# Performance work log

Measured on AMD Instinct MI355X. Metric: run time of the kernel, lower is better.

## Reference

```python
import jax, jax.numpy as jnp
import numpy as np


def setup_inputs() -> dict:
    key = jax.random.key(0)
    k0, k1, k2, k3 = jax.random.split(key, 4)
    H = 256  # hidden_dim_size
    DK = 256
    DV = 256
    hidden_states = jax.random.normal(k0, (1, 32, H, 16, 16), dtype=jnp.float32)
    # torch nn.Linear(H, dk, bias=False) computes x @ W.T; we store W.T directly as (H, dk)
    Wq = jax.random.normal(k1, (H, DK), dtype=jnp.float32) * (1.0 / np.sqrt(H))
    Wk = jax.random.normal(k2, (H, DK), dtype=jnp.float32) * (1.0 / np.sqrt(H))
    Wv = jax.random.normal(k3, (H, DV), dtype=jnp.float32) * (1.0 / np.sqrt(H))
    return {"hidden_states": hidden_states, "Wq": Wq, "Wk": Wk, "Wv": Wv}


def reference(hidden_states, Wq, Wk, Wv):
    # (b, t, c, h, w) -> (b, t, h, w, c)
    x = jnp.transpose(hidden_states, (0, 1, 3, 4, 2))
    nb, nt, nr, nc, nh = x.shape
    xf = x.reshape(-1, nh)  # (N, H) with N = b*t*h*w
    q = xf @ Wq             # (N, dk)
    k = xf @ Wk             # (N, dk)
    v = xf @ Wv             # (N, dv)
    dk = Wq.shape[1]
    scores = (q @ k.T) / jnp.sqrt(jnp.asarray(dk, dtype=q.dtype))  # (N, N)
    attn = jax.nn.softmax(scores, axis=-1) @ v                     # (N, dv)
    out = attn.reshape(nb, nt, nr, nc, -1)
    return jnp.transpose(out, (0, 1, 4, 2, 3))  # (b, t, dv, h, w)
```

## Files before the change

kernel.cpp:

```cpp
#include <hip/hip_runtime.h>
#include <stdint.h>

typedef __attribute__((ext_vector_type(8))) short bh8;
typedef __attribute__((ext_vector_type(4))) float f32x4;
typedef __attribute__((ext_vector_type(16))) float f32x16;
typedef __attribute__((ext_vector_type(2))) __fp16 h16x2;
typedef unsigned int uint32;

__device__ __forceinline__ unsigned short f2bf(float f) {
  uint32 u = __builtin_bit_cast(uint32, f);
  u += 0x7fffu + ((u >> 16) & 1u);
  return (unsigned short)(u >> 16);
}

__device__ __forceinline__ uint32 cvtpk_bf16(float lo, float hi) {
  uint32 r;
  asm("v_cvt_pk_bf16_f32 %0, %1, %2" : "=v"(r) : "v"(lo), "v"(hi));
  return r;
}

__device__ __forceinline__ float exp2_hw(float x) {
  float r;
  asm("v_exp_f32 %0, %1" : "=v"(r) : "v"(x));
  return r;
}

__device__ __forceinline__ float max3f(float a, float b, float c) {
  return fmaxf(fmaxf(a, b), c);
}

__device__ __forceinline__ void lds_load16(const void* g, void* l) {
  auto gp = (const __attribute__((address_space(1))) uint32*)(uintptr_t)(g);
  auto lp = (__attribute__((address_space(3))) uint32*)(uintptr_t)(l);
  __builtin_amdgcn_global_load_lds(gp, lp, 16, 0, 0);
}

__global__ __launch_bounds__(256) void k_transpose(
    const float* __restrict__ hidden, const float* __restrict__ Wq,
    const float* __restrict__ Wk, const float* __restrict__ Wv,
    unsigned short* __restrict__ xb, unsigned short* __restrict__ wt) {
  int bid = blockIdx.x, c0 = blockIdx.y * 16, tid = threadIdx.x;
  const float* in; unsigned short* out; float scale = 1.0f;
  if (bid < 32) { in = hidden + (size_t)bid * 65536; out = xb + (size_t)bid * 65536; }
  else {
    int j = bid - 32;
    in = (j == 0) ? Wq : (j == 1 ? Wk : Wv);
    out = wt + (size_t)j * 65536;
    if (j == 0) scale = 0.0625f * 1.4426950408889634f;
  }
  __shared__ uint32 lt[256 * 9];
  uint32 pk[8];
#pragma unroll
  for (int i = 0; i < 8; ++i) {
    float a = in[(size_t)(c0 + 2 * i) * 256 + tid] * scale;
    float b = in[(size_t)(c0 + 2 * i + 1) * 256 + tid] * scale;
    pk[i] = (uint32)f2bf(a) | ((uint32)f2bf(b) << 16);
  }
#pragma unroll
  for (int i = 0; i < 8; ++i) lt[tid * 9 + i] = pk[i];
  __syncthreads();
  int q2 = tid & 1;
#pragma unroll
  for (int rr = 0; rr < 2; ++rr) {
    int r = rr * 128 + (tid >> 1);
    uint4 v;
    v.x = lt[r * 9 + q2 * 4 + 0]; v.y = lt[r * 9 + q2 * 4 + 1];
    v.z = lt[r * 9 + q2 * 4 + 2]; v.w = lt[r * 9 + q2 * 4 + 3];
    *(uint4*)(out + (size_t)r * 256 + c0 + q2 * 8) = v;
  }
}

__global__ __launch_bounds__(256, 2) void k_gemm(
    const unsigned short* __restrict__ xb, const unsigned short* __restrict__ wt,
    unsigned short* __restrict__ qb, unsigned short* __restrict__ kb,
    unsigned short* __restrict__ vtb) {
  __shared__ char lds[32768];
  char* ldsA = lds; char* ldsB = lds + 16384;
  int tid = threadIdx.x, z = blockIdx.z;
  int l = tid & 63, w = tid >> 6, g = l >> 4, r15 = l & 15;
  int wr = w >> 1, wc = w & 1;
  const unsigned short *Ag, *Bg; unsigned short* out;
  int arow0, brow0; size_t ostride;
  if (z < 2) {
    Ag = xb; arow0 = blockIdx.x * 128;
    Bg = wt + (size_t)z * 65536; brow0 = blockIdx.y * 128;
    out = z ? kb : qb; ostride = 256;
  } else {
    Ag = wt + 2 * 65536; arow0 = blockIdx.y * 128;
    Bg = xb; brow0 = blockIdx.x * 128;
    out = vtb; ostride = 8192;
  }
  f32x4 acc[4][4];
#pragma unroll
  for (int i = 0; i < 4; ++i)
#pragma unroll
    for (int j = 0; j < 4; ++j) acc[i][j] = (f32x4){0.f, 0.f, 0.f, 0.f};

  for (int kk = 0; kk < 4; ++kk) {
    int c0 = kk * 64;
    __syncthreads();
#pragma unroll
    for (int p = 0; p < 4; ++p) {
      int off = p * 4096 + tid * 16;
      int row = off >> 7, ch = (off >> 4) & 7, sc = ch ^ (row & 7);
      lds_load16((const char*)Ag + ((size_t)(arow0 + row) * 256 + c0) * 2 + sc * 16, ldsA + off);
    }
#pragma unroll
    for (int p = 0; p < 4; ++p) {
      int off = p * 4096 + tid * 16;
      int row = off >> 7, ch = (off >> 4) & 7, sc = ch ^ (row & 7);
      lds_load16((const char*)Bg + ((size_t)(brow0 + row) * 256 + c0) * 2 + sc * 16, ldsB + off);
    }
    __syncthreads();
#pragma unroll
    for (int ks = 0; ks < 2; ++ks) {
      bh8 af[4], bfr[4];
#pragma unroll
      for (int i = 0; i < 4; ++i) {
        int rowa = wr * 64 + i * 16 + r15;
        af[i] = *(const bh8*)(ldsA + rowa * 128 + (((ks * 4 + g) ^ (rowa & 7)) * 16));
        int rowb = wc * 64 + i * 16 + r15;
        bfr[i] = *(const bh8*)(ldsB + rowb * 128 + (((ks * 4 + g) ^ (rowb & 7)) * 16));
      }
#pragma unroll
      for (int i = 0; i < 4; ++i)
#pragma unroll
        for (int j = 0; j < 4; ++j)
          acc[i][j] = __builtin_amdgcn_mfma_f32_16x16x32_bf16(af[i], bfr[j], acc[i][j], 0, 0, 0);
    }
  }
  __syncthreads();
#pragma unroll
  for (int i = 0; i < 4; ++i)
#pragma unroll
    for (int j = 0; j < 4; ++j)
#pragma unroll
      for (int r = 0; r < 4; ++r) {
        int rowl = wr * 64 + i * 16 + g * 4 + r;
        int coll = wc * 64 + j * 16 + r15;
        *(unsigned short*)(lds + rowl * 256 + coll * 2) = f2bf(acc[i][j][r]);
      }
  __syncthreads();
#pragma unroll
  for (int p = 0; p < 8; ++p) {
    int off = p * 4096 + tid * 16;
    int row = off >> 8, colb = off & 255;
    *(uint4*)((char*)out + ((size_t)(arow0 + row) * ostride + (size_t)brow0) * 2 + colb) =
        *(const uint4*)(lds + off);
  }
}

__global__ __launch_bounds__(512, 2) void k_attn(
    const unsigned short* __restrict__ qg, const unsigned short* __restrict__ kg,
    const unsigned short* __restrict__ vtg, uint32* __restrict__ Op,
    float* __restrict__ mp, float* __restrict__ lp, int S, int shift, int KS) {
  extern __shared__ char smem[];
  int tid = threadIdx.x;
  int w = tid >> 6, l = tid & 63, col = l & 31, half = l >> 5;
  int bid = blockIdx.x;
  int s = bid & (S - 1);
  int qb = bid >> shift;
  int qrow0 = qb * 256 + w * 32;

  int nt = KS >> 6, kb0 = s * KS;

  auto stage = [&](int buf, int kvb) {
    char* Kd = smem + buf * 65536;
    char* Vd = Kd + 32768;
#pragma unroll
    for (int p = 0; p < 4; ++p) {
      int off = p * 8192 + tid * 16;
      int row = off >> 9, ch = (off >> 4) & 31;
      lds_load16((const char*)kg + (size_t)(kvb + row) * 512 + ((ch ^ (row & 7)) * 16), Kd + off);
    }
#pragma unroll
    for (int p = 0; p < 4; ++p) {
      int off = p * 8192 + tid * 16;
      int row = off >> 7, ch = (off >> 4) & 7;
      lds_load16((const char*)vtg + (size_t)row * 16384 + (size_t)kvb * 2 + ((ch ^ (row & 7)) * 16),
                 Vd + off);
    }
  };

  stage(0, kb0);

  bh8 qf[16];
  {
    const char* qrow = (const char*)qg + (size_t)(qrow0 + col) * 512 + half * 16;
#pragma unroll
    for (int t = 0; t < 16; ++t) qf[t] = *(const bh8*)(qrow + t * 32);
  }

  f32x16 o[8];
#pragma unroll
  for (int dt = 0; dt < 8; ++dt)
#pragma unroll
    for (int i = 0; i < 16; ++i) o[dt][i] = 0.f;
  float m = -INFINITY, ls = 0.f;

  for (int kt = 0; kt < nt; ++kt) {
    int cur = kt & 1;
    if (kt + 1 < nt) {
      stage(cur ^ 1, kb0 + (kt + 1) * 64);
      asm volatile("s_waitcnt vmcnt(8)" ::: "memory");
    } else {
      asm volatile("s_waitcnt vmcnt(0)" ::: "memory");
    }
    __builtin_amdgcn_s_barrier();
    char* Kl = smem + cur * 65536;
    char* Vl = Kl + 32768;

    f32x16 sc0, sc1;
#pragma unroll
    for (int i = 0; i < 16; ++i) { sc0[i] = 0.f; sc1[i] = 0.f; }
    int r0 = col, r1 = 32 + col;
#pragma unroll
    for (int t = 0; t < 16; ++t) {
      bh8 kf0 = *(const bh8*)(Kl + r0 * 512 + (((2 * t + half) ^ (r0 & 7)) * 16));
      bh8 kf1 = *(const bh8*)(Kl + r1 * 512 + (((2 * t + half) ^ (r1 & 7)) * 16));
      sc0 = __builtin_amdgcn_mfma_f32_32x32x16_bf16(kf0, qf[t], sc0, 0, 0, 0);
      sc1 = __builtin_amdgcn_mfma_f32_32x32x16_bf16(kf1, qf[t], sc1, 0, 0, 0);
    }

    float t0 = max3f(sc0[0], sc0[1], sc0[2]);
    float t1 = max3f(sc0[3], sc0[4], sc0[5]);
    float t2 = max3f(sc0[6], sc0[7], sc0[8]);
    float t3 = max3f(sc0[9], sc0[10], sc0[11]);
    float t4 = max3f(sc0[12], sc0[13], sc0[14]);
    float rm0 = fmaxf(max3f(t0, t1, t2), max3f(t3, t4, sc0[15]));
    float u0 = max3f(sc1[0], sc1[1], sc1[2]);
    float u1 = max3f(sc1[3], sc1[4], sc1[5]);
    float u2 = max3f(sc1[6], sc1[7], sc1[8]);
    float u3 = max3f(sc1[9], sc1[10], sc1[11]);
    float u4 = max3f(sc1[12], sc1[13], sc1[14]);
    float rm1 = fmaxf(max3f(u0, u1, u2), max3f(u3, u4, sc1[15]));
    float rm = fmaxf(rm0, rm1);
    rm = fmaxf(rm, __shfl_xor(rm, 32));

    if (__any(rm > m + 6.0f)) {
      float mn = fmaxf(m, rm);
      float scl = exp2_hw(m - mn);
      m = mn;
      float sclb[16];
#pragma unroll
      for (int i = 0; i < 16; ++i) {
        int qs = (i & 3) + 8 * (i >> 2) + 4 * half;
        sclb[i] = __shfl(scl, qs);
      }
#pragma unroll
      for (int dt = 0; dt < 8; ++dt)
#pragma unroll
        for (int i = 0; i < 16; ++i) o[dt][i] *= sclb[i];
      ls *= scl;
    }
#pragma unroll
    for (int i = 0; i < 16; ++i) sc0[i] = exp2_hw(sc0[i] - m);
#pragma unroll
    for (int i = 0; i < 16; ++i) sc1[i] = exp2_hw(sc1[i] - m);
    float s0 = ((sc0[0] + sc0[1]) + (sc0[2] + sc0[3])) + ((sc0[4] + sc0[5]) + (sc0[6] + sc0[7]));
    float s1 = ((sc0[8] + sc0[9]) + (sc0[10] + sc0[11])) + ((sc0[12] + sc0[13]) + (sc0[14] + sc0[15]));
    float s2 = ((sc1[0] + sc1[1]) + (sc1[2] + sc1[3])) + ((sc1[4] + sc1[5]) + (sc1[6] + sc1[7]));
    float s3 = ((sc1[8] + sc1[9]) + (sc1[10] + sc1[11])) + ((sc1[12] + sc1[13]) + (sc1[14] + sc1[15]));
    float rsum = (s0 + s1) + (s2 + s3);
    rsum += __shfl_xor(rsum, 32);
    ls += rsum;

    bh8 pa[4];
#pragma unroll
    for (int t2 = 0; t2 < 2; ++t2) {
      const f32x16& p = t2 ? sc1 : sc0;
      uint32 c0 = cvtpk_bf16(p[0], p[1]),   c1 = cvtpk_bf16(p[2], p[3]);
      uint32 c2 = cvtpk_bf16(p[4], p[5]),   c3 = cvtpk_bf16(p[6], p[7]);
      uint32 c4 = cvtpk_bf16(p[8], p[9]),   c5 = cvtpk_bf16(p[10], p[11]);
      uint32 c6 = cvtpk_bf16(p[12], p[13]), c7 = cvtpk_bf16(p[14], p[15]);
      uint32 za = half ? c0 : c2, zb = half ? c1 : c3;
      uint32 zc = half ? c4 : c6, zd = half ? c5 : c7;
      za = __shfl_xor((int)za, 32); zb = __shfl_xor((int)zb, 32);
      zc = __shfl_xor((int)zc, 32); zd = __shfl_xor((int)zd, 32);
      uint4 v0, v1;
      if (half == 0) { v0 = (uint4){c0, c1, za, zb}; v1 = (uint4){c4, c5, zc, zd}; }
      else           { v0 = (uint4){za, zb, c2, c3}; v1 = (uint4){zc, zd, c6, c7}; }
      pa[2 * t2 + 0] = __builtin_bit_cast(bh8, v0);
      pa[2 * t2 + 1] = __builtin_bit_cast(bh8, v1);
    }

#pragma unroll
    for (int dt = 0; dt < 8; ++dt) {
      int rv = dt * 32 + col;
#pragma unroll
      for (int ks = 0; ks < 4; ++ks) {
        bh8 vf = *(const bh8*)(Vl + rv * 128 + (((2 * ks + half) ^ (rv & 7)) * 16));
        o[dt] = __builtin_amdgcn_mfma_f32_32x32x16_bf16(pa[ks], vf, o[dt], 0, 0, 0);
      }
    }

    __builtin_amdgcn_s_barrier();
  }

#pragma unroll
  for (int i = 0; i < 16; ++i) {
    int qr = (i & 3) + 8 * (i >> 2) + 4 * half;
    uint32* ob = Op + ((size_t)s * 8192 + qrow0 + qr) * 128 + col;
#pragma unroll
    for (int j = 0; j < 4; ++j) {
      h16x2 hp = __builtin_amdgcn_cvt_pkrtz(o[2 * j][i], o[2 * j + 1][i]);
      ob[j * 32] = __builtin_bit_cast(uint32, hp);
    }
  }
  if (l < 32) {
    mp[(size_t)s * 8192 + qrow0 + col] = m;
    lp[(size_t)s * 8192 + qrow0 + col] = ls;
  }
}

__global__ __launch_bounds__(256) void k_combine(
    const uint32* __restrict__ Op, const float* __restrict__ mp,
    const float* __restrict__ lp, float* __restrict__ out, int S) {
  __shared__ float wsc[16 * 128];
  __shared__ float lt[64 * 129];
  int t = blockIdx.x, j = blockIdx.y, ph = blockIdx.z, tid = threadIdx.x;
  int n0 = t * 256 + ph * 128;

  if (tid < 128) {
    int n = n0 + tid;
    float mt = -INFINITY;
#pragma unroll 16
    for (int s = 0; s < 16; ++s)
      if (s < S) mt = fmaxf(mt, mp[(size_t)s * 8192 + n]);
    float den = 0.f;
#pragma unroll 16
    for (int s = 0; s < 16; ++s)
      if (s < S) den += exp2f(mp[(size_t)s * 8192 + n] - mt) * lp[(size_t)s * 8192 + n];
    float inv = 1.0f / den;
#pragma unroll 16
    for (int s = 0; s < 16; ++s)
      if (s < S) wsc[s * 128 + tid] = exp2f(mp[(size_t)s * 8192 + n] - mt) * inv;
  }
  __syncthreads();

  int c = tid & 31, rg = tid >> 5;
  for (int pass = 0; pass < 16; ++pass) {
    int p = pass * 8 + rg;
    int n = n0 + p;
    float alo = 0.f, ahi = 0.f;
#pragma unroll 16
    for (int s = 0; s < 16; ++s)
      if (s < S) {
        uint32 v = Op[((size_t)s * 8192 + n) * 128 + j * 32 + c];
        h16x2 h2 = __builtin_bit_cast(h16x2, v);
        float ws = wsc[s * 128 + p];
        alo += ws * (float)h2[0];
        ahi += ws * (float)h2[1];
      }
    lt[c * 129 + p] = alo;
    lt[(c + 32) * 129 + p] = ahi;
  }
  __syncthreads();

  int dd = tid >> 2, pq = tid & 3;
  float* ob = out + (size_t)t * 65536 + (size_t)(j * 64 + dd) * 256 + ph * 128 + pq * 32;
  const float* lr = &lt[dd * 129 + pq * 32];
#pragma unroll
  for (int i = 0; i < 8; ++i) {
    float4 v;
    v.x = lr[4 * i + 0]; v.y = lr[4 * i + 1]; v.z = lr[4 * i + 2]; v.w = lr[4 * i + 3];
    *(float4*)(ob + 4 * i) = v;
  }
}

extern "C" void kernel_launch(void* const* d_in, const int* in_sizes, int n_in,
                              void* d_out, int out_size, void* d_ws, size_t ws_size,
                              hipStream_t stream) {
  const float* hidden = (const float*)d_in[0];
  const float* Wq = (const float*)d_in[1];
  const float* Wk = (const float*)d_in[2];
  const float* Wv = (const float*)d_in[3];
  float* out = (float*)d_out;
  char* ws = (char*)d_ws;

  const size_t off_x  = 0;
  const size_t off_wt = 4ull << 20;
  const size_t off_q  = off_wt + 3ull * 131072;
  const size_t off_k  = off_q + 8192ull * 256 * 2;
  const size_t off_vt = off_k + 8192ull * 256 * 2;
  const size_t off_O  = off_vt + 8192ull * 256 * 2;

  int S = 8, shift = 3;
  {
    auto need = [&](int s) { return off_O + (size_t)s * 8192 * 128 * 4; };
    if (ws_size < need(8)) { S = 4; shift = 2; }
    if (ws_size < need(4)) { S = 2; shift = 1; }
  }

  unsigned short* xb  = (unsigned short*)(ws + off_x);
  unsigned short* wt  = (unsigned short*)(ws + off_wt);
  unsigned short* qb  = (unsigned short*)(ws + off_q);
  unsigned short* kb  = (unsigned short*)(ws + off_k);
  unsigned short* vtb = (unsigned short*)(ws + off_vt);
  uint32* Op = (uint32*)(ws + off_O);
  float* mp = (float*)(ws + off_x);
  float* lp = (float*)(ws + off_x + (2ull << 20));
  int KS = 8192 / S;

  const int attn_lds = 131072;
  (void)hipFuncSetAttribute((const void*)k_attn, hipFuncAttributeMaxDynamicSharedMemorySize,
                            attn_lds);

  k_transpose<<<dim3(35, 16), dim3(256), 0, stream>>>(hidden, Wq, Wk, Wv, xb, wt);
  k_gemm<<<dim3(64, 2, 3), dim3(256), 0, stream>>>(xb, wt, qb, kb, vtb);
  k_attn<<<dim3(32 * S), dim3(512), attn_lds, stream>>>(qb, kb, vtb, Op, mp, lp, S, shift, KS);
  k_combine<<<dim3(32, 4, 2), dim3(256), 0, stream>>>(Op, mp, lp, out, S);
}
```

Before: 161.9 us.

## Give each attention wave 64 query rows to reuse K/V fragments

The attention kernel drops from 8 to 4 waves per block. Each wave now owns 64 query rows as two 32-row groups and processes the 64-key tile in two 32-key halves. Each K and V fragment read from LDS now feeds two MFMAs, which halves LDS read traffic per MFMA. The cost is roughly double the accumulator and Q register footprint (two 8x16-float O sets plus 32 Q fragments), which likely forces one block per CU at launch bounds (256,1). That could hurt latency hiding or cause register spills.

New measurement: 623.2 us. +284.9%, slower.

```diff
diff --git a/kernel.cpp b/kernel.cpp
--- a/kernel.cpp
+++ b/kernel.cpp
@@ -150,7 +150,7 @@
   }
 }
 
-__global__ __launch_bounds__(512, 2) void k_attn(
+__global__ __launch_bounds__(256, 1) void k_attn(
     const unsigned short* __restrict__ qg, const unsigned short* __restrict__ kg,
     const unsigned short* __restrict__ vtg, uint32* __restrict__ Op,
     float* __restrict__ mp, float* __restrict__ lp, int S, int shift, int KS) {
@@ -160,7 +160,7 @@
   int bid = blockIdx.x;
   int s = bid & (S - 1);
   int qb = bid >> shift;
-  int qrow0 = qb * 256 + w * 32;
+  int qrow0 = qb * 256 + w * 64;
 
   int nt = KS >> 6, kb0 = s * KS;
 
@@ -168,14 +168,14 @@
     char* Kd = smem + buf * 65536;
     char* Vd = Kd + 32768;
 #pragma unroll
-    for (int p = 0; p < 4; ++p) {
-      int off = p * 8192 + tid * 16;
+    for (int p = 0; p < 8; ++p) {
+      int off = p * 4096 + tid * 16;
       int row = off >> 9, ch = (off >> 4) & 31;
       lds_load16((const char*)kg + (size_t)(kvb + row) * 512 + ((ch ^ (row & 7)) * 16), Kd + off);
     }
 #pragma unroll
-    for (int p = 0; p < 4; ++p) {
-      int off = p * 8192 + tid * 16;
+    for (int p = 0; p < 8; ++p) {
+      int off = p * 4096 + tid * 16;
       int row = off >> 7, ch = (off >> 4) & 7;
       lds_load16((const char*)vtg + (size_t)row * 16384 + (size_t)kvb * 2 + ((ch ^ (row & 7)) * 16),
                  Vd + off);
@@ -184,25 +184,28 @@
 
   stage(0, kb0);
 
-  bh8 qf[16];
+  bh8 qf0[16], qf1[16];
   {
     const char* qrow = (const char*)qg + (size_t)(qrow0 + col) * 512 + half * 16;
 #pragma unroll
-    for (int t = 0; t < 16; ++t) qf[t] = *(const bh8*)(qrow + t * 32);
-  }
-
-  f32x16 o[8];
+    for (int t = 0; t < 16; ++t) qf0[t] = *(const bh8*)(qrow + t * 32);
+    const char* qrow1 = qrow + 32 * 512;
+#pragma unroll
+    for (int t = 0; t < 16; ++t) qf1[t] = *(const bh8*)(qrow1 + t * 32);
+  }
+
+  f32x16 o0[8], o1[8];
 #pragma unroll
   for (int dt = 0; dt < 8; ++dt)
 #pragma unroll
-    for (int i = 0; i < 16; ++i) o[dt][i] = 0.f;
-  float m = -INFINITY, ls = 0.f;
+    for (int i = 0; i < 16; ++i) { o0[dt][i] = 0.f; o1[dt][i] = 0.f; }
+  float m0 = -INFINITY, ls0 = 0.f, m1 = -INFINITY, ls1 = 0.f;
 
   for (int kt = 0; kt < nt; ++kt) {
     int cur = kt & 1;
     if (kt + 1 < nt) {
       stage(cur ^ 1, kb0 + (kt + 1) * 64);
-      asm volatile("s_waitcnt vmcnt(8)" ::: "memory");
+      asm volatile("s_waitcnt vmcnt(16)" ::: "memory");
     } else {
       asm volatile("s_waitcnt vmcnt(0)" ::: "memory");
     }
@@ -210,87 +213,92 @@
     char* Kl = smem + cur * 65536;
     char* Vl = Kl + 32768;
 
-    f32x16 sc0, sc1;
-#pragma unroll
-    for (int i = 0; i < 16; ++i) { sc0[i] = 0.f; sc1[i] = 0.f; }
-    int r0 = col, r1 = 32 + col;
-#pragma unroll
-    for (int t = 0; t < 16; ++t) {
-      bh8 kf0 = *(const bh8*)(Kl + r0 * 512 + (((2 * t + half) ^ (r0 & 7)) * 16));
-      bh8 kf1 = *(const bh8*)(Kl + r1 * 512 + (((2 * t + half) ^ (r1 & 7)) * 16));
-      sc0 = __builtin_amdgcn_mfma_f32_32x32x16_bf16(kf0, qf[t], sc0, 0, 0, 0);
-      sc1 = __builtin_amdgcn_mfma_f32_32x32x16_bf16(kf1, qf[t], sc1, 0, 0, 0);
-    }
-
-    float t0 = max3f(sc0[0], sc0[1], sc0[2]);
-    float t1 = max3f(sc0[3], sc0[4], sc0[5]);
-    float t2 = max3f(sc0[6], sc0[7], sc0[8]);
-    float t3 = max3f(sc0[9], sc0[10], sc0[11]);
-    float t4 = max3f(sc0[12], sc0[13], sc0[14]);
-    float rm0 = fmaxf(max3f(t0, t1, t2), max3f(t3, t4, sc0[15]));
-    float u0 = max3f(sc1[0], sc1[1], sc1[2]);
-    float u1 = max3f(sc1[3], sc1[4], sc1[5]);
-    float u2 = max3f(sc1[6], sc1[7], sc1[8]);
-    float u3 = max3f(sc1[9], sc1[10], sc1[11]);
-    float u4 = max3f(sc1[12], sc1[13], sc1[14]);
-    float rm1 = fmaxf(max3f(u0, u1, u2), max3f(u3, u4, sc1[15]));
-    float rm = fmaxf(rm0, rm1);
-    rm = fmaxf(rm, __shfl_xor(rm, 32));
-
-    if (__any(rm > m + 6.0f)) {
-      float mn = fmaxf(m, rm);
-      float scl = exp2_hw(m - mn);
-      m = mn;
-      float sclb[16];
-#pragma unroll
-      for (int i = 0; i < 16; ++i) {
-        int qs = (i & 3) + 8 * (i >> 2) + 4 * half;
-        sclb[i] = __shfl(scl, qs);
-      }
-#pragma unroll
-      for (int dt = 0; dt < 8; ++dt)
-#pragma unroll
-        for (int i = 0; i < 16; ++i) o[dt][i] *= sclb[i];
-      ls *= scl;
-    }
-#pragma unroll
-    for (int i = 0; i < 16; ++i) sc0[i] = exp2_hw(sc0[i] - m);
-#pragma unroll
-    for (int i = 0; i < 16; ++i) sc1[i] = exp2_hw(sc1[i] - m);
-    float s0 = ((sc0[0] + sc0[1]) + (sc0[2] + sc0[3])) + ((sc0[4] + sc0[5]) + (sc0[6] + sc0[7]));
-    float s1 = ((sc0[8] + sc0[9]) + (sc0[10] + sc0[11])) + ((sc0[12] + sc0[13]) + (sc0[14] + sc0[15]));
-    float s2 = ((sc1[0] + sc1[1]) + (sc1[2] + sc1[3])) + ((sc1[4] + sc1[5]) + (sc1[6] + sc1[7]));
-    float s3 = ((sc1[8] + sc1[9]) + (sc1[10] + sc1[11])) + ((sc1[12] + sc1[13]) + (sc1[14] + sc1[15]));
-    float rsum = (s0 + s1) + (s2 + s3);
-    rsum += __shfl_xor(rsum, 32);
-    ls += rsum;
-
-    bh8 pa[4];
-#pragma unroll
-    for (int t2 = 0; t2 < 2; ++t2) {
-      const f32x16& p = t2 ? sc1 : sc0;
-      uint32 c0 = cvtpk_bf16(p[0], p[1]),   c1 = cvtpk_bf16(p[2], p[3]);
-      uint32 c2 = cvtpk_bf16(p[4], p[5]),   c3 = cvtpk_bf16(p[6], p[7]);
-      uint32 c4 = cvtpk_bf16(p[8], p[9]),   c5 = cvtpk_bf16(p[10], p[11]);
-      uint32 c6 = cvtpk_bf16(p[12], p[13]), c7 = cvtpk_bf16(p[14], p[15]);
-      uint32 za = half ? c0 : c2, zb = half ? c1 : c3;
-      uint32 zc = half ? c4 : c6, zd = half ? c5 : c7;
-      za = __shfl_xor((int)za, 32); zb = __shfl_xor((int)zb, 32);
-      zc = __shfl_xor((int)zc, 32); zd = __shfl_xor((int)zd, 32);
-      uint4 v0, v1;
-      if (half == 0) { v0 = (uint4){c0, c1, za, zb}; v1 = (uint4){c4, c5, zc, zd}; }
-      else           { v0 = (uint4){za, zb, c2, c3}; v1 = (uint4){zc, zd, c6, c7}; }
-      pa[2 * t2 + 0] = __builtin_bit_cast(bh8, v0);
-      pa[2 * t2 + 1] = __builtin_bit_cast(bh8, v1);
-    }
-
-#pragma unroll
-    for (int dt = 0; dt < 8; ++dt) {
-      int rv = dt * 32 + col;
-#pragma unroll
-      for (int ks = 0; ks < 4; ++ks) {
-        bh8 vf = *(const bh8*)(Vl + rv * 128 + (((2 * ks + half) ^ (rv & 7)) * 16));
-        o[dt] = __builtin_amdgcn_mfma_f32_32x32x16_bf16(pa[ks], vf, o[dt], 0, 0, 0);
+#pragma unroll
+    for (int kh = 0; kh < 2; ++kh) {
+      int krow = kh * 32 + col;
+
+      f32x16 sc0, sc1;
+#pragma unroll
+      for (int i = 0; i < 16; ++i) { sc0[i] = 0.f; sc1[i] = 0.f; }
+#pragma unroll
+      for (int t = 0; t < 16; ++t) {
+        bh8 kf = *(const bh8*)(Kl + krow * 512 + (((2 * t + half) ^ (krow & 7)) * 16));
+        sc0 = __builtin_amdgcn_mfma_f32_32x32x16_bf16(kf, qf0[t], sc0, 0, 0, 0);
+        sc1 = __builtin_amdgcn_mfma_f32_32x32x16_bf16(kf, qf1[t], sc1, 0, 0, 0);
+      }
+
+      float a0 = max3f(sc0[0], sc0[1], sc0[2]);
+      float a1 = max3f(sc0[3], sc0[4], sc0[5]);
+      float a2 = max3f(sc0[6], sc0[7], sc0[8]);
+      float a3 = max3f(sc0[9], sc0[10], sc0[11]);
+      float a4 = max3f(sc0[12], sc0[13], sc0[14]);
+      float rm0 = fmaxf(max3f(a0, a1, a2), max3f(a3, a4, sc0[15]));
+      float b0 = max3f(sc1[0], sc1[1], sc1[2]);
+      float b1 = max3f(sc1[3], sc1[4], sc1[5]);
+      float b2 = max3f(sc1[6], sc1[7], sc1[8]);
+      float b3 = max3f(sc1[9], sc1[10], sc1[11]);
+      float b4 = max3f(sc1[12], sc1[13], sc1[14]);
+      float rm1 = fmaxf(max3f(b0, b1, b2), max3f(b3, b4, sc1[15]));
+      rm0 = fmaxf(rm0, __shfl_xor(rm0, 32));
+      rm1 = fmaxf(rm1, __shfl_xor(rm1, 32));
+
+      if (__any(rm0 > m0 + 6.0f || rm1 > m1 + 6.0f)) {
+        float mn0 = fmaxf(m0, rm0), mn1 = fmaxf(m1, rm1);
+        float scl0 = exp2_hw(m0 - mn0), scl1 = exp2_hw(m1 - mn1);
+        m0 = mn0; m1 = mn1;
+        float sb0[16], sb1[16];
+#pragma unroll
+        for (int i = 0; i < 16; ++i) {
+          int qs = (i & 3) + 8 * (i >> 2) + 4 * half;
+          sb0[i] = __shfl(scl0, qs);
+          sb1[i] = __shfl(scl1, qs);
+        }
+#pragma unroll
+        for (int dt = 0; dt < 8; ++dt)
+#pragma unroll
+          for (int i = 0; i < 16; ++i) { o0[dt][i] *= sb0[i]; o1[dt][i] *= sb1[i]; }
+        ls0 *= scl0; ls1 *= scl1;
+      }
+#pragma unroll
+      for (int i = 0; i < 16; ++i) { sc0[i] = exp2_hw(sc0[i] - m0); sc1[i] = exp2_hw(sc1[i] - m1); }
+      float p0 = ((sc0[0] + sc0[1]) + (sc0[2] + sc0[3])) + ((sc0[4] + sc0[5]) + (sc0[6] + sc0[7]));
+      float p1 = ((sc0[8] + sc0[9]) + (sc0[10] + sc0[11])) + ((sc0[12] + sc0[13]) + (sc0[14] + sc0[15]));
+      float rs0 = p0 + p1;
+      float p2 = ((sc1[0] + sc1[1]) + (sc1[2] + sc1[3])) + ((sc1[4] + sc1[5]) + (sc1[6] + sc1[7]));
+      float p3 = ((sc1[8] + sc1[9]) + (sc1[10] + sc1[11])) + ((sc1[12] + sc1[13]) + (sc1[14] + sc1[15]));
+      float rs1 = p2 + p3;
+      rs0 += __shfl_xor(rs0, 32);
+      rs1 += __shfl_xor(rs1, 32);
+      ls0 += rs0; ls1 += rs1;
+
+      bh8 pa0[2], pa1[2];
+#pragma unroll
+      for (int t2 = 0; t2 < 2; ++t2) {
+        const f32x16& p = t2 ? sc1 : sc0;
+        uint32 c0 = cvtpk_bf16(p[0], p[1]),   c1 = cvtpk_bf16(p[2], p[3]);
+        uint32 c2 = cvtpk_bf16(p[4], p[5]),   c3 = cvtpk_bf16(p[6], p[7]);
+        uint32 c4 = cvtpk_bf16(p[8], p[9]),   c5 = cvtpk_bf16(p[10], p[11]);
+        uint32 c6 = cvtpk_bf16(p[12], p[13]), c7 = cvtpk_bf16(p[14], p[15]);
+        uint32 za = half ? c0 : c2, zb = half ? c1 : c3;
+        uint32 zc = half ? c4 : c6, zd = half ? c5 : c7;
+        za = __shfl_xor((int)za, 32); zb = __shfl_xor((int)zb, 32);
+        zc = __shfl_xor((int)zc, 32); zd = __shfl_xor((int)zd, 32);
+        uint4 v0, v1;
+        if (half == 0) { v0 = (uint4){c0, c1, za, zb}; v1 = (uint4){c4, c5, zc, zd}; }
+        else           { v0 = (uint4){za, zb, c2, c3}; v1 = (uint4){zc, zd, c6, c7}; }
+        if (t2 == 0) { pa0[0] = __builtin_bit_cast(bh8, v0); pa0[1] = __builtin_bit_cast(bh8, v1); }
+        else         { pa1[0] = __builtin_bit_cast(bh8, v0); pa1[1] = __builtin_bit_cast(bh8, v1); }
+      }
+
+#pragma unroll
+      for (int dt = 0; dt < 8; ++dt) {
+        int rv = dt * 32 + col;
+#pragma unroll
+        for (int ks = 0; ks < 2; ++ks) {
+          bh8 vf = *(const bh8*)(Vl + rv * 128 + (((kh * 4 + 2 * ks + half) ^ (rv & 7)) * 16));
+          o0[dt] = __builtin_amdgcn_mfma_f32_32x32x16_bf16(ks ? pa0[1] : pa0[0], vf, o0[dt], 0, 0, 0);
+          o1[dt] = __builtin_amdgcn_mfma_f32_32x32x16_bf16(ks ? pa1[1] : pa1[0], vf, o1[dt], 0, 0, 0);
+        }
       }
     }
 
@@ -300,16 +308,21 @@
 #pragma unroll
   for (int i = 0; i < 16; ++i) {
     int qr = (i & 3) + 8 * (i >> 2) + 4 * half;
-    uint32* ob = Op + ((size_t)s * 8192 + qrow0 + qr) * 128 + col;
+    uint32* ob0 = Op + ((size_t)s * 8192 + qrow0 + qr) * 128 + col;
+    uint32* ob1 = Op + ((size_t)s * 8192 + qrow0 + 32 + qr) * 128 + col;
 #pragma unroll
     for (int j = 0; j < 4; ++j) {
-      h16x2 hp = __builtin_amdgcn_cvt_pkrtz(o[2 * j][i], o[2 * j + 1][i]);
-      ob[j * 32] = __builtin_bit_cast(uint32, hp);
+      h16x2 hp0 = __builtin_amdgcn_cvt_pkrtz(o0[2 * j][i], o0[2 * j + 1][i]);
+      h16x2 hp1 = __builtin_amdgcn_cvt_pkrtz(o1[2 * j][i], o1[2 * j + 1][i]);
+      ob0[j * 32] = __builtin_bit_cast(uint32, hp0);
+      ob1[j * 32] = __builtin_bit_cast(uint32, hp1);
     }
   }
   if (l < 32) {
-    mp[(size_t)s * 8192 + qrow0 + col] = m;
-    lp[(size_t)s * 8192 + qrow0 + col] = ls;
+    mp[(size_t)s * 8192 + qrow0 + col] = m0;
+    lp[(size_t)s * 8192 + qrow0 + col] = ls0;
+    mp[(size_t)s * 8192 + qrow0 + 32 + col] = m1;
+    lp[(size_t)s * 8192 + qrow0 + 32 + col] = ls1;
   }
 }
 
@@ -408,6 +421,6 @@
 
   k_transpose<<<dim3(35, 16), dim3(256), 0, stream>>>(hidden, Wq, Wk, Wv, xb, wt);
   k_gemm<<<dim3(64, 2, 3), dim3(256), 0, stream>>>(xb, wt, qb, kb, vtb);
-  k_attn<<<dim3(32 * S), dim3(512), attn_lds, stream>>>(qb, kb, vtb, Op, mp, lp, S, shift, KS);
+  k_attn<<<dim3(32 * S), dim3(256), attn_lds, stream>>>(qb, kb, vtb, Op, mp, lp, S, shift, KS);
   k_combine<<<dim3(32, 4, 2), dim3(256), 0, stream>>>(Op, mp, lp, out, S);
 }
```

## Software-pipeline attention: overlap QK^T of next tile with PV of previous tile

Applied to the files above, without the earlier changes.

Restructures the flash-attention loop so the QK^T MFMAs for tile kt are interleaved with the PV MFMAs for tile kt-1, with softmax of tile kt running after both. This exposes independent MFMA chains alongside softmax work within each wave. V moves to a triple-buffered LDS ring, and K keeps a double buffer. LDS use rises to 160KB per block. Each iteration now waits for all outstanding loads with vmcnt(0) and drops the trailing barrier.

New measurement: 164.8 us. About the same (+1.8%).

```diff
diff --git a/kernel.cpp b/kernel.cpp
--- a/kernel.cpp
+++ b/kernel.cpp
@@ -164,15 +164,21 @@
 
   int nt = KS >> 6, kb0 = s * KS;
 
-  auto stage = [&](int buf, int kvb) {
-    char* Kd = smem + buf * 65536;
-    char* Vd = Kd + 32768;
+  char* Kb0 = smem;
+  char* Kb1 = smem + 32768;
+  char* Vp = smem + 65536 + 2 * 32768;
+  char* Vc = smem + 65536;
+  char* Vn = smem + 65536 + 32768;
+
+  auto stageK = [&](char* Kd, int kvb) {
 #pragma unroll
     for (int p = 0; p < 4; ++p) {
       int off = p * 8192 + tid * 16;
       int row = off >> 9, ch = (off >> 4) & 31;
       lds_load16((const char*)kg + (size_t)(kvb + row) * 512 + ((ch ^ (row & 7)) * 16), Kd + off);
     }
+  };
+  auto stageV = [&](char* Vd, int kvb) {
 #pragma unroll
     for (int p = 0; p < 4; ++p) {
       int off = p * 8192 + tid * 16;
@@ -182,7 +188,8 @@
     }
   };
 
-  stage(0, kb0);
+  stageK(Kb0, kb0);
+  stageV(Vc, kb0);
 
   bh8 qf[16];
   {
@@ -197,31 +204,10 @@
 #pragma unroll
     for (int i = 0; i < 16; ++i) o[dt][i] = 0.f;
   float m = -INFINITY, ls = 0.f;
-
-  for (int kt = 0; kt < nt; ++kt) {
-    int cur = kt & 1;
-    if (kt + 1 < nt) {
-      stage(cur ^ 1, kb0 + (kt + 1) * 64);
-      asm volatile("s_waitcnt vmcnt(8)" ::: "memory");
-    } else {
-      asm volatile("s_waitcnt vmcnt(0)" ::: "memory");
-    }
-    __builtin_amdgcn_s_barrier();
-    char* Kl = smem + cur * 65536;
-    char* Vl = Kl + 32768;
-
-    f32x16 sc0, sc1;
-#pragma unroll
-    for (int i = 0; i < 16; ++i) { sc0[i] = 0.f; sc1[i] = 0.f; }
-    int r0 = col, r1 = 32 + col;
-#pragma unroll
-    for (int t = 0; t < 16; ++t) {
-      bh8 kf0 = *(const bh8*)(Kl + r0 * 512 + (((2 * t + half) ^ (r0 & 7)) * 16));
-      bh8 kf1 = *(const bh8*)(Kl + r1 * 512 + (((2 * t + half) ^ (r1 & 7)) * 16));
-      sc0 = __builtin_amdgcn_mfma_f32_32x32x16_bf16(kf0, qf[t], sc0, 0, 0, 0);
-      sc1 = __builtin_amdgcn_mfma_f32_32x32x16_bf16(kf1, qf[t], sc1, 0, 0, 0);
-    }
-
+  bh8 pa[4];
+  int r0 = col, r1 = 32 + col;
+
+  auto softmax_pa = [&](f32x16& sc0, f32x16& sc1) {
     float t0 = max3f(sc0[0], sc0[1], sc0[2]);
     float t1 = max3f(sc0[3], sc0[4], sc0[5]);
     float t2 = max3f(sc0[6], sc0[7], sc0[8]);
@@ -265,7 +251,6 @@
     rsum += __shfl_xor(rsum, 32);
     ls += rsum;
 
-    bh8 pa[4];
 #pragma unroll
     for (int t2 = 0; t2 < 2; ++t2) {
       const f32x16& p = t2 ? sc1 : sc0;
@@ -283,18 +268,63 @@
       pa[2 * t2 + 0] = __builtin_bit_cast(bh8, v0);
       pa[2 * t2 + 1] = __builtin_bit_cast(bh8, v1);
     }
-
-#pragma unroll
-    for (int dt = 0; dt < 8; ++dt) {
+  };
+
+  {
+    asm volatile("s_waitcnt vmcnt(0)" ::: "memory");
+    __builtin_amdgcn_s_barrier();
+    if (nt > 1) { stageK(Kb1, kb0 + 64); stageV(Vn, kb0 + 64); }
+    char* Kl = Kb0;
+    f32x16 sc0, sc1;
+#pragma unroll
+    for (int i = 0; i < 16; ++i) { sc0[i] = 0.f; sc1[i] = 0.f; }
+#pragma unroll
+    for (int t = 0; t < 16; ++t) {
+      bh8 kf0 = *(const bh8*)(Kl + r0 * 512 + (((2 * t + half) ^ (r0 & 7)) * 16));
+      bh8 kf1 = *(const bh8*)(Kl + r1 * 512 + (((2 * t + half) ^ (r1 & 7)) * 16));
+      sc0 = __builtin_amdgcn_mfma_f32_32x32x16_bf16(kf0, qf[t], sc0, 0, 0, 0);
+      sc1 = __builtin_amdgcn_mfma_f32_32x32x16_bf16(kf1, qf[t], sc1, 0, 0, 0);
+    }
+    softmax_pa(sc0, sc1);
+    char* tmp = Vp; Vp = Vc; Vc = Vn; Vn = tmp;
+  }
+
+  for (int kt = 1; kt < nt; ++kt) {
+    asm volatile("s_waitcnt vmcnt(0)" ::: "memory");
+    __builtin_amdgcn_s_barrier();
+    if (kt + 1 < nt) {
+      stageK((kt & 1) ? Kb0 : Kb1, kb0 + (kt + 1) * 64);
+      stageV(Vn, kb0 + (kt + 1) * 64);
+    }
+    char* Kl = (kt & 1) ? Kb1 : Kb0;
+    f32x16 sc0, sc1;
+#pragma unroll
+    for (int i = 0; i < 16; ++i) { sc0[i] = 0.f; sc1[i] = 0.f; }
+#pragma unroll
+    for (int t = 0; t < 16; ++t) {
+      bh8 kf0 = *(const bh8*)(Kl + r0 * 512 + (((2 * t + half) ^ (r0 & 7)) * 16));
+      bh8 kf1 = *(const bh8*)(Kl + r1 * 512 + (((2 * t + half) ^ (r1 & 7)) * 16));
+      sc0 = __builtin_amdgcn_mfma_f32_32x32x16_bf16(kf0, qf[t], sc0, 0, 0, 0);
+      sc1 = __builtin_amdgcn_mfma_f32_32x32x16_bf16(kf1, qf[t], sc1, 0, 0, 0);
+      int dt = t >> 1, ksb = (t & 1) * 2;
       int rv = dt * 32 + col;
-#pragma unroll
-      for (int ks = 0; ks < 4; ++ks) {
-        bh8 vf = *(const bh8*)(Vl + rv * 128 + (((2 * ks + half) ^ (rv & 7)) * 16));
-        o[dt] = __builtin_amdgcn_mfma_f32_32x32x16_bf16(pa[ks], vf, o[dt], 0, 0, 0);
-      }
-    }
-
-    __builtin_amdgcn_s_barrier();
+      bh8 vfa = *(const bh8*)(Vp + rv * 128 + (((2 * ksb + half) ^ (rv & 7)) * 16));
+      o[dt] = __builtin_amdgcn_mfma_f32_32x32x16_bf16(pa[ksb], vfa, o[dt], 0, 0, 0);
+      bh8 vfb = *(const bh8*)(Vp + rv * 128 + (((2 * ksb + 2 + half) ^ (rv & 7)) * 16));
+      o[dt] = __builtin_amdgcn_mfma_f32_32x32x16_bf16(pa[ksb + 1], vfb, o[dt], 0, 0, 0);
+    }
+    softmax_pa(sc0, sc1);
+    char* tmp = Vp; Vp = Vc; Vc = Vn; Vn = tmp;
+  }
+
+#pragma unroll
+  for (int dt = 0; dt < 8; ++dt) {
+    int rv = dt * 32 + col;
+#pragma unroll
+    for (int ks = 0; ks < 4; ++ks) {
+      bh8 vf = *(const bh8*)(Vp + rv * 128 + (((2 * ks + half) ^ (rv & 7)) * 16));
+      o[dt] = __builtin_amdgcn_mfma_f32_32x32x16_bf16(pa[ks], vf, o[dt], 0, 0, 0);
+    }
   }
 
 #pragma unroll
@@ -402,7 +432,7 @@
   float* lp = (float*)(ws + off_x + (2ull << 20));
   int KS = 8192 / S;
 
-  const int attn_lds = 131072;
+  const int attn_lds = 163840;
   (void)hipFuncSetAttribute((const void*)k_attn, hipFuncAttributeMaxDynamicSharedMemorySize,
                             attn_lds);
 
```
